# Optimization experiments

Measured on AMD Instinct MI355X. Metric: run time of the kernel, lower is better.

Reference implementation:

```python
import jax, jax.numpy as jnp
import numpy as np

ALPHA = 0.3
B, T, I, H = 256, 1024, 128, 1024


def setup_inputs() -> dict:
    key = jax.random.key(0)
    ks = jax.random.split(key, 7)
    s = 1.0 / np.sqrt(H)
    return {
        "x": jax.random.normal(ks[0], (B, T, I), dtype=jnp.float32),
        "W_ih": jax.random.normal(ks[1], (3 * H, I), dtype=jnp.float32) * s,
        "W_hh": jax.random.normal(ks[2], (3 * H, H), dtype=jnp.float32) * s,
        "b_ih": jax.random.normal(ks[3], (3 * H,), dtype=jnp.float32) * s,
        "b_hh": jax.random.normal(ks[4], (3 * H,), dtype=jnp.float32) * s,
        "W_fc": jax.random.normal(ks[5], (2, H), dtype=jnp.float32) * s,
        "b_fc": jax.random.normal(ks[6], (2,), dtype=jnp.float32) * s,
    }


def _forward(x, W_ih, W_hh, b_ih, b_hh, W_fc, b_fc):
    # --- ES normalize: s_i = (1-a)*x_i + a*s_{i-1}, s_0 = x_0 (in-place EMA) ---
    xs = jnp.swapaxes(x, 0, 1)  # [T, B, I]
    s0 = xs[0]

    def ema_step(s, xi):
        s2 = (1.0 - ALPHA) * xi + ALPHA * s
        return s2, s2

    _, rest = jax.lax.scan(ema_step, s0, xs[1:])
    sm = jnp.concatenate([s0[None], rest], axis=0)  # [T, B, I] smoothed
    st_1 = sm[-1]  # [B, I]

    # --- GRU (single layer, batch_first, h0 = 0); gate order r, z, n ---
    gi = jnp.einsum('tbi,gi->tbg', sm, W_ih) + b_ih  # [T, B, 3H]
    h0 = jnp.zeros((x.shape[0], W_hh.shape[1]), dtype=x.dtype)

    def gru_step(h, gi_t):
        gh = h @ W_hh.T + b_hh  # [B, 3H]
        i_r, i_z, i_n = jnp.split(gi_t, 3, axis=-1)
        h_r, h_z, h_n = jnp.split(gh, 3, axis=-1)
        r = jax.nn.sigmoid(i_r + h_r)
        z = jax.nn.sigmoid(i_z + h_z)
        n = jnp.tanh(i_n + r * h_n)
        h2 = (1.0 - z) * n + z * h
        return h2, None

    h_out, _ = jax.lax.scan(gru_step, h0, gi)  # [B, H]

    out = h_out @ W_fc.T + b_fc  # [B, 2]
    # --- ES denormalize with columns [1, 2] of st_1 ---
    out = (out - ALPHA * st_1[:, 1:3]) / (1.0 - ALPHA)
    return out


def reference(x, W_ih, W_hh, b_ih, b_hh, W_fc, b_fc):
    return _forward(x, W_ih, W_hh, b_ih, b_hh, W_fc, b_fc)
```

## Files before the change

kernel.cpp:

```cpp
#include <hip/hip_runtime.h>

typedef __attribute__((ext_vector_type(4))) float f4;
typedef __attribute__((ext_vector_type(8))) short frag8;
typedef unsigned long long u64;
typedef unsigned int u32;
typedef unsigned short u16;

#define ALPHA 0.3f

#define WHH_OFF   0ull
#define WIH_OFF   6291456ull
#define HBUF_OFF  7077888ull
#define FLG_OFF   8126464ull
#define ST1_OFF   8128512ull
#define ZERO_LEN  1052672ull

__device__ __forceinline__ u16 f2bf(float f) {
  u32 u = __float_as_uint(f);
  u32 r = (u + 0x7FFFu + ((u >> 16) & 1u)) >> 16;
  return (u16)r;
}
__device__ __forceinline__ float bf2f(u16 h) {
  return __uint_as_float(((u32)h) << 16);
}
__device__ __forceinline__ float sigmf(float x) {
  float e = __expf(-fabsf(x));
  float s = 1.0f / (1.0f + e);
  return x >= 0.f ? s : 1.0f - s;
}
__device__ __forceinline__ float tanhf_(float x) {
  float e = __expf(-2.0f * fabsf(x));
  float t = (1.0f - e) / (1.0f + e);
  return x >= 0.f ? t : -t;
}
__device__ __forceinline__ frag8 pack_bf16(f4 a, f4 b) {
  union { u16 h[8]; frag8 f; } u;
  u.h[0] = f2bf(a[0]); u.h[1] = f2bf(a[1]); u.h[2] = f2bf(a[2]); u.h[3] = f2bf(a[3]);
  u.h[4] = f2bf(b[0]); u.h[5] = f2bf(b[1]); u.h[6] = f2bf(b[2]); u.h[7] = f2bf(b[3]);
  return u.f;
}

__global__ void prep_bf16(const float* __restrict__ whh_f32,
                          const float* __restrict__ wih_f32,
                          u16* __restrict__ whh, u16* __restrict__ wih) {
  int i = blockIdx.x * 256 + threadIdx.x;
  const int nhh = 3072 * 1024;
  if (i < nhh) whh[i] = f2bf(whh_f32[i]);
  else         wih[i - nhh] = f2bf(wih_f32[i - nhh]);
}

__global__ __launch_bounds__(256, 1) void gru_kernel(
    const float* __restrict__ x,
    const float* __restrict__ b_ih,
    const float* __restrict__ b_hh,
    const u16* __restrict__ whh,
    const u16* __restrict__ wih,
    u64* __restrict__ hbuf,
    u32* __restrict__ flags,
    float* __restrict__ st1)
{
  __shared__ f4 xbuf[4096];
  __shared__ u16 sbuf[32 * 40];
  const int wg = blockIdx.x;
  const int g = wg >> 5, w = wg & 31;
  const int tid = threadIdx.x;
  const int v = tid >> 6;
  const int l = tid & 63;
  const int lm = l & 15, lq = l >> 4;

  frag8 whhf[8][6];
  frag8 wihf[6];
#pragma unroll
  for (int rt = 0; rt < 6; ++rt) {
    int grow = (rt >> 1) * 1024 + w * 32 + (rt & 1) * 16 + lm;
    wihf[rt] = *(const frag8*)(wih + grow * 128 + v * 32 + lq * 8);
#pragma unroll
    for (int kb = 0; kb < 8; ++kb)
      whhf[kb][rt] = *(const frag8*)(whh + grow * 1024 + v * 256 + kb * 32 + lq * 8);
  }

  const int uc = tid & 31;
  const int ub0 = (tid >> 5) << 2;
  const int colg = w * 32 + uc;
  const float bir = b_ih[colg],         bhr = b_hh[colg];
  const float biz = b_ih[1024 + colg],  bhz = b_hh[1024 + colg];
  const float bin_ = b_ih[2048 + colg], bhn = b_hh[2048 + colg];
  f4 hprev = {0.f, 0.f, 0.f, 0.f};

  f4 e0a, e0b, e1a, e1b;
  const float* xb0 = x + (size_t)(g * 32 + lm) * 131072 + v * 32 + lq * 8;
  const float* xb1 = x + (size_t)(g * 32 + 16 + lm) * 131072 + v * 32 + lq * 8;

  u32* fbase = flags + g * 64;
  const f4 zz = {0.f, 0.f, 0.f, 0.f};
  const float A1 = 1.0f - ALPHA;

  f4 acc[2][6], accn[2][2];

  auto gi_compute = [&](int tt) {
    const float* xp0 = xb0 + (size_t)tt * 128;
    const float* xp1 = xb1 + (size_t)tt * 128;
    f4 xa0 = *(const f4*)xp0, xc0 = *(const f4*)(xp0 + 4);
    f4 xa1 = *(const f4*)xp1, xc1 = *(const f4*)(xp1 + 4);
    if (tt == 0) { e0a = xa0; e0b = xc0; e1a = xa1; e1b = xc1; }
    else {
      e0a = A1 * xa0 + ALPHA * e0a; e0b = A1 * xc0 + ALPHA * e0b;
      e1a = A1 * xa1 + ALPHA * e1a; e1b = A1 * xc1 + ALPHA * e1b;
    }
    frag8 smf0 = pack_bf16(e0a, e0b);
    frag8 smf1 = pack_bf16(e1a, e1b);
#pragma unroll
    for (int bh = 0; bh < 2; ++bh) {
#pragma unroll
      for (int rt = 0; rt < 6; ++rt) acc[bh][rt] = zz;
      accn[bh][0] = zz; accn[bh][1] = zz;
    }
#pragma unroll
    for (int rt = 0; rt < 4; ++rt) {
      acc[0][rt] = __builtin_amdgcn_mfma_f32_16x16x32_bf16(smf0, wihf[rt], acc[0][rt], 0, 0, 0);
      acc[1][rt] = __builtin_amdgcn_mfma_f32_16x16x32_bf16(smf1, wihf[rt], acc[1][rt], 0, 0, 0);
    }
#pragma unroll
    for (int nt = 0; nt < 2; ++nt) {
      accn[0][nt] = __builtin_amdgcn_mfma_f32_16x16x32_bf16(smf0, wihf[4 + nt], accn[0][nt], 0, 0, 0);
      accn[1][nt] = __builtin_amdgcn_mfma_f32_16x16x32_bf16(smf1, wihf[4 + nt], accn[1][nt], 0, 0, 0);
    }
  };

  gi_compute(0);

#pragma unroll 1
  for (int t = 0; t < 1024; ++t) {
    u64* hread  = hbuf + (size_t)((t & 1) * 8 + g) * 8192;
    u64* hwrite = hbuf + (size_t)(((t + 1) & 1) * 8 + g) * 8192;

    frag8 af[8][2];
#pragma unroll
    for (int kb = 0; kb < 8; ++kb) {
#pragma unroll
      for (int bh = 0; bh < 2; ++bh) {
        int base = (((8 * v + kb) * 2 + bh) * 64 + l) * 2;
        union { u64 q[2]; frag8 f; } uu;
        uu.q[0] = __hip_atomic_load(hread + base,     __ATOMIC_RELAXED, __HIP_MEMORY_SCOPE_AGENT);
        uu.q[1] = __hip_atomic_load(hread + base + 1, __ATOMIC_RELAXED, __HIP_MEMORY_SCOPE_AGENT);
        af[kb][bh] = uu.f;
      }
    }
#pragma unroll
    for (int kb = 0; kb < 8; ++kb) {
#pragma unroll
      for (int rt = 0; rt < 6; ++rt) {
        acc[0][rt] = __builtin_amdgcn_mfma_f32_16x16x32_bf16(af[kb][0], whhf[kb][rt], acc[0][rt], 0, 0, 0);
        acc[1][rt] = __builtin_amdgcn_mfma_f32_16x16x32_bf16(af[kb][1], whhf[kb][rt], acc[1][rt], 0, 0, 0);
      }
    }

#pragma unroll
    for (int bh = 0; bh < 2; ++bh) {
      int b8 = bh * 4 + lq;
#pragma unroll
      for (int rt = 0; rt < 6; ++rt) {
        int gr = rt * 16 + lm;
        xbuf[((v * 128 + gr) << 3) | (b8 ^ (gr & 7))] = acc[bh][rt];
      }
#pragma unroll
      for (int nt = 0; nt < 2; ++nt) {
        int gr = 96 + nt * 16 + lm;
        xbuf[((v * 128 + gr) << 3) | (b8 ^ (gr & 7))] = accn[bh][nt];
      }
    }
    __syncthreads();

    int swz = (ub0 >> 2) ^ (uc & 7);
    f4 sr = zz, sz4 = zz, gn4 = zz, gin4 = zz;
#pragma unroll
    for (int vv = 0; vv < 4; ++vv) {
      sr   += xbuf[((vv * 128 + uc) << 3) | swz];
      sz4  += xbuf[((vv * 128 + 32 + uc) << 3) | swz];
      gn4  += xbuf[((vv * 128 + 64 + uc) << 3) | swz];
      gin4 += xbuf[((vv * 128 + 96 + uc) << 3) | swz];
    }
    f4 h4;
#pragma unroll
    for (int i = 0; i < 4; ++i) {
      float rr = sigmf(sr[i] + bir + bhr);
      float zg = sigmf(sz4[i] + biz + bhz);
      float nn = tanhf_(gin4[i] + bin_ + rr * (gn4[i] + bhn));
      h4[i] = (1.0f - zg) * nn + zg * hprev[i];
    }
    hprev = h4;

#pragma unroll
    for (int i = 0; i < 4; ++i) sbuf[(ub0 + i) * 40 + uc] = f2bf(h4[i]);
    __syncthreads();
    {
      int b = tid >> 3, c0 = (tid & 7) << 2;
      u64 pk = *(const u64*)(sbuf + b * 40 + c0);
      int off = ((w * 2 + (b >> 4)) * 64 + (b & 15) + 16 * (c0 >> 3)) * 2 + ((c0 & 7) >> 2);
      __hip_atomic_store(hwrite + off, pk, __ATOMIC_RELAXED, __HIP_MEMORY_SCOPE_AGENT);
    }
    __syncthreads();

    if (tid == 0)
      __hip_atomic_store(fbase + w, (u32)(t + 1), __ATOMIC_RELEASE, __HIP_MEMORY_SCOPE_AGENT);

    if (t < 1023) gi_compute(t + 1);

    if (v == 0) {
      u32 tgt = (u32)(t + 1);
      for (;;) {
        u32 f = __hip_atomic_load(fbase + (l & 31), __ATOMIC_RELAXED, __HIP_MEMORY_SCOPE_AGENT);
        if (__ballot(f < tgt) == 0) break;
        __builtin_amdgcn_s_sleep(1);
      }
      __builtin_amdgcn_fence(__ATOMIC_ACQUIRE, "agent");
    }
    __syncthreads();
  }

  if (w == 0 && v == 0 && lq == 0) {
    st1[(g * 32 + lm) * 2 + 0] = e0a[1];
    st1[(g * 32 + lm) * 2 + 1] = e0a[2];
    st1[(g * 32 + 16 + lm) * 2 + 0] = e1a[1];
    st1[(g * 32 + 16 + lm) * 2 + 1] = e1a[2];
  }
}

__global__ void fc_kernel(const u16* __restrict__ hbuf_bf,
                          const float* __restrict__ wfc,
                          const float* __restrict__ bfc,
                          const float* __restrict__ st1,
                          float* __restrict__ out)
{
  int b = blockIdx.x, t = threadIdx.x;
  int g = b >> 5, bl = b & 31, bh = bl >> 4;
  int k0 = t * 4, kb = k0 >> 5, ko = k0 & 31;
  int lane = (bl & 15) + 16 * (ko >> 3);
  const u16* hp = hbuf_bf + (size_t)g * 32768 + ((kb * 2 + bh) * 64 + lane) * 8 + (ko & 7);
  float h0 = bf2f(hp[0]), h1 = bf2f(hp[1]), h2 = bf2f(hp[2]), h3 = bf2f(hp[3]);
  float s0 = h0 * wfc[k0] + h1 * wfc[k0 + 1] + h2 * wfc[k0 + 2] + h3 * wfc[k0 + 3];
  float s1 = h0 * wfc[1024 + k0] + h1 * wfc[1024 + k0 + 1] +
             h2 * wfc[1024 + k0 + 2] + h3 * wfc[1024 + k0 + 3];
#pragma unroll
  for (int off = 32; off > 0; off >>= 1) {
    s0 += __shfl_down(s0, off);
    s1 += __shfl_down(s1, off);
  }
  __shared__ float red[8];
  if ((t & 63) == 0) { red[(t >> 6) * 2] = s0; red[(t >> 6) * 2 + 1] = s1; }
  __syncthreads();
  if (t == 0) {
    float a0 = red[0] + red[2] + red[4] + red[6] + bfc[0];
    float a1 = red[1] + red[3] + red[5] + red[7] + bfc[1];
    float inv = 1.0f / (1.0f - ALPHA);
    out[b * 2 + 0] = (a0 - ALPHA * st1[b * 2 + 0]) * inv;
    out[b * 2 + 1] = (a1 - ALPHA * st1[b * 2 + 1]) * inv;
  }
}

extern "C" void kernel_launch(void* const* d_in, const int* in_sizes, int n_in,
                              void* d_out, int out_size, void* d_ws, size_t ws_size,
                              hipStream_t stream) {
  const float* x   = (const float*)d_in[0];
  const float* Wih = (const float*)d_in[1];
  const float* Whh = (const float*)d_in[2];
  const float* bih = (const float*)d_in[3];
  const float* bhh = (const float*)d_in[4];
  const float* Wfc = (const float*)d_in[5];
  const float* bfc = (const float*)d_in[6];
  char* ws = (char*)d_ws;
  u16* whh_bf = (u16*)(ws + WHH_OFF);
  u16* wih_bf = (u16*)(ws + WIH_OFF);
  u64* hbuf   = (u64*)(ws + HBUF_OFF);
  u32* flags  = (u32*)(ws + FLG_OFF);
  float* st1  = (float*)(ws + ST1_OFF);

  hipMemsetAsync(ws + HBUF_OFF, 0, ZERO_LEN, stream);
  prep_bf16<<<13824, 256, 0, stream>>>(Whh, Wih, whh_bf, wih_bf);
  gru_kernel<<<256, 256, 0, stream>>>(x, bih, bhh, whh_bf, wih_bf, hbuf, flags, st1);
  fc_kernel<<<256, 256, 0, stream>>>((const u16*)(ws + HBUF_OFF), Wfc, bfc, st1,
                                     (float*)d_out);
}
```

Baseline: 11.53 ms.

## Replace block barrier handoff with per-wave flags and row-major hidden-state layout

The end-of-step barrier handoff is replaced: each wave now publishes its own release flag right after storing its share of the new hidden state, and every wave polls per-wave flags at the start of the next step. The second __syncthreads and the single-thread flag store are gone. The input projection is now computed at the top of each step, before the wait, and the next x row is prefetched. The hidden buffer moves to a plain row-major bf16 layout with 32-bit stores, and fc_kernel reads it accordingly. The aim is to cut barrier latency on the serial recurrence critical path. The risk is 4x more flags to poll, and the acquire fence is replaced by only a compiler barrier, which may weaken memory ordering.

```diff
diff --git a/kernel.cpp b/kernel.cpp
--- a/kernel.cpp
+++ b/kernel.cpp
@@ -12,7 +12,7 @@
 #define WIH_OFF   6291456ull
 #define HBUF_OFF  7077888ull
 #define FLG_OFF   8126464ull
-#define ST1_OFF   8128512ull
+#define ST1_OFF   8130560ull
 #define ZERO_LEN  1052672ull
 
 __device__ __forceinline__ u16 f2bf(float f) {
@@ -55,12 +55,12 @@
     const float* __restrict__ b_hh,
     const u16* __restrict__ whh,
     const u16* __restrict__ wih,
-    u64* __restrict__ hbuf,
+    u16* __restrict__ hbuf,
     u32* __restrict__ flags,
     float* __restrict__ st1)
 {
   __shared__ f4 xbuf[4096];
-  __shared__ u16 sbuf[32 * 40];
+  __shared__ u16 sbuf[1024];
   const int wg = blockIdx.x;
   const int g = wg >> 5, w = wg & 31;
   const int tid = threadIdx.x;
@@ -90,25 +90,32 @@
   f4 e0a, e0b, e1a, e1b;
   const float* xb0 = x + (size_t)(g * 32 + lm) * 131072 + v * 32 + lq * 8;
   const float* xb1 = x + (size_t)(g * 32 + 16 + lm) * 131072 + v * 32 + lq * 8;
-
-  u32* fbase = flags + g * 64;
+  f4 xn0 = *(const f4*)xb0, xn1 = *(const f4*)(xb0 + 4);
+  f4 xn2 = *(const f4*)xb1, xn3 = *(const f4*)(xb1 + 4);
+
+  u32* flg = flags + g * 128;
+  const u32 fidx = v * 32 + (l & 31);
+  const float A1 = 1.0f - ALPHA;
   const f4 zz = {0.f, 0.f, 0.f, 0.f};
-  const float A1 = 1.0f - ALPHA;
-
   f4 acc[2][6], accn[2][2];
 
-  auto gi_compute = [&](int tt) {
-    const float* xp0 = xb0 + (size_t)tt * 128;
-    const float* xp1 = xb1 + (size_t)tt * 128;
-    f4 xa0 = *(const f4*)xp0, xc0 = *(const f4*)(xp0 + 4);
-    f4 xa1 = *(const f4*)xp1, xc1 = *(const f4*)(xp1 + 4);
-    if (tt == 0) { e0a = xa0; e0b = xc0; e1a = xa1; e1b = xc1; }
+#pragma unroll 1
+  for (int t = 0; t < 1024; ++t) {
+    const u64* hr64 = (const u64*)(hbuf + (size_t)((t & 1) * 8 + g) * 32768);
+    u32* hw32 = (u32*)(hbuf + (size_t)(((t + 1) & 1) * 8 + g) * 32768);
+
+    if (t == 0) { e0a = xn0; e0b = xn1; e1a = xn2; e1b = xn3; }
     else {
-      e0a = A1 * xa0 + ALPHA * e0a; e0b = A1 * xc0 + ALPHA * e0b;
-      e1a = A1 * xa1 + ALPHA * e1a; e1b = A1 * xc1 + ALPHA * e1b;
+      e0a = A1 * xn0 + ALPHA * e0a; e0b = A1 * xn1 + ALPHA * e0b;
+      e1a = A1 * xn2 + ALPHA * e1a; e1b = A1 * xn3 + ALPHA * e1b;
     }
     frag8 smf0 = pack_bf16(e0a, e0b);
     frag8 smf1 = pack_bf16(e1a, e1b);
+    {
+      size_t to = (size_t)(t < 1023 ? t + 1 : 1023) * 128;
+      xn0 = *(const f4*)(xb0 + to); xn1 = *(const f4*)(xb0 + to + 4);
+      xn2 = *(const f4*)(xb1 + to); xn3 = *(const f4*)(xb1 + to + 4);
+    }
 #pragma unroll
     for (int bh = 0; bh < 2; ++bh) {
 #pragma unroll
@@ -125,24 +132,26 @@
       accn[0][nt] = __builtin_amdgcn_mfma_f32_16x16x32_bf16(smf0, wihf[4 + nt], accn[0][nt], 0, 0, 0);
       accn[1][nt] = __builtin_amdgcn_mfma_f32_16x16x32_bf16(smf1, wihf[4 + nt], accn[1][nt], 0, 0, 0);
     }
-  };
-
-  gi_compute(0);
-
-#pragma unroll 1
-  for (int t = 0; t < 1024; ++t) {
-    u64* hread  = hbuf + (size_t)((t & 1) * 8 + g) * 8192;
-    u64* hwrite = hbuf + (size_t)(((t + 1) & 1) * 8 + g) * 8192;
+
+    {
+      const u32 tgt = (u32)t;
+      for (;;) {
+        u32 f = __hip_atomic_load(flg + fidx, __ATOMIC_RELAXED, __HIP_MEMORY_SCOPE_AGENT);
+        if (__ballot(f < tgt) == 0ull) break;
+        __builtin_amdgcn_s_sleep(2);
+      }
+      asm volatile("" ::: "memory");
+    }
 
     frag8 af[8][2];
 #pragma unroll
     for (int kb = 0; kb < 8; ++kb) {
 #pragma unroll
       for (int bh = 0; bh < 2; ++bh) {
-        int base = (((8 * v + kb) * 2 + bh) * 64 + l) * 2;
+        const u64* p = hr64 + (bh * 16 + lm) * 256 + (v * 8 + kb) * 8 + lq * 2;
         union { u64 q[2]; frag8 f; } uu;
-        uu.q[0] = __hip_atomic_load(hread + base,     __ATOMIC_RELAXED, __HIP_MEMORY_SCOPE_AGENT);
-        uu.q[1] = __hip_atomic_load(hread + base + 1, __ATOMIC_RELAXED, __HIP_MEMORY_SCOPE_AGENT);
+        uu.q[0] = __hip_atomic_load(p,     __ATOMIC_RELAXED, __HIP_MEMORY_SCOPE_AGENT);
+        uu.q[1] = __hip_atomic_load(p + 1, __ATOMIC_RELAXED, __HIP_MEMORY_SCOPE_AGENT);
         af[kb][bh] = uu.f;
       }
     }
@@ -189,33 +198,20 @@
       h4[i] = (1.0f - zg) * nn + zg * hprev[i];
     }
     hprev = h4;
-
-#pragma unroll
-    for (int i = 0; i < 4; ++i) sbuf[(ub0 + i) * 40 + uc] = f2bf(h4[i]);
+#pragma unroll
+    for (int i = 0; i < 4; ++i) sbuf[(ub0 + i) * 32 + uc] = f2bf(h4[i]);
     __syncthreads();
+
     {
-      int b = tid >> 3, c0 = (tid & 7) << 2;
-      u64 pk = *(const u64*)(sbuf + b * 40 + c0);
-      int off = ((w * 2 + (b >> 4)) * 64 + (b & 15) + 16 * (c0 >> 3)) * 2 + ((c0 & 7) >> 2);
-      __hip_atomic_store(hwrite + off, pk, __ATOMIC_RELAXED, __HIP_MEMORY_SCOPE_AGENT);
-    }
-    __syncthreads();
-
-    if (tid == 0)
-      __hip_atomic_store(fbase + w, (u32)(t + 1), __ATOMIC_RELEASE, __HIP_MEMORY_SCOPE_AGENT);
-
-    if (t < 1023) gi_compute(t + 1);
-
-    if (v == 0) {
-      u32 tgt = (u32)(t + 1);
-      for (;;) {
-        u32 f = __hip_atomic_load(fbase + (l & 31), __ATOMIC_RELAXED, __HIP_MEMORY_SCOPE_AGENT);
-        if (__ballot(f < tgt) == 0) break;
-        __builtin_amdgcn_s_sleep(1);
-      }
-      __builtin_amdgcn_fence(__ATOMIC_ACQUIRE, "agent");
-    }
-    __syncthreads();
+      const u32* s32 = (const u32*)sbuf;
+      u32 a0 = s32[tid], a1 = s32[tid + 256];
+      int b0 = tid >> 4,        c0 = tid & 15;
+      int b1 = (tid + 256) >> 4, c1 = tid & 15;
+      __hip_atomic_store(hw32 + b0 * 512 + w * 16 + c0, a0, __ATOMIC_RELAXED, __HIP_MEMORY_SCOPE_AGENT);
+      __hip_atomic_store(hw32 + b1 * 512 + w * 16 + c1, a1, __ATOMIC_RELAXED, __HIP_MEMORY_SCOPE_AGENT);
+      if (l == 0)
+        __hip_atomic_store(flg + w * 4 + v, (u32)(t + 1), __ATOMIC_RELEASE, __HIP_MEMORY_SCOPE_AGENT);
+    }
   }
 
   if (w == 0 && v == 0 && lq == 0) {
@@ -226,18 +222,18 @@
   }
 }
 
-__global__ void fc_kernel(const u16* __restrict__ hbuf_bf,
+__global__ void fc_kernel(const u16* __restrict__ hbuf,
                           const float* __restrict__ wfc,
                           const float* __restrict__ bfc,
                           const float* __restrict__ st1,
                           float* __restrict__ out)
 {
   int b = blockIdx.x, t = threadIdx.x;
-  int g = b >> 5, bl = b & 31, bh = bl >> 4;
-  int k0 = t * 4, kb = k0 >> 5, ko = k0 & 31;
-  int lane = (bl & 15) + 16 * (ko >> 3);
-  const u16* hp = hbuf_bf + (size_t)g * 32768 + ((kb * 2 + bh) * 64 + lane) * 8 + (ko & 7);
-  float h0 = bf2f(hp[0]), h1 = bf2f(hp[1]), h2 = bf2f(hp[2]), h3 = bf2f(hp[3]);
+  int g = b >> 5, bl = b & 31;
+  int k0 = t * 4;
+  u64 hv = ((const u64*)(hbuf + (size_t)g * 32768))[bl * 256 + t];
+  float h0 = bf2f((u16)(hv & 0xFFFF)),         h1 = bf2f((u16)((hv >> 16) & 0xFFFF));
+  float h2 = bf2f((u16)((hv >> 32) & 0xFFFF)), h3 = bf2f((u16)(hv >> 48));
   float s0 = h0 * wfc[k0] + h1 * wfc[k0 + 1] + h2 * wfc[k0 + 2] + h3 * wfc[k0 + 3];
   float s1 = h0 * wfc[1024 + k0] + h1 * wfc[1024 + k0 + 1] +
              h2 * wfc[1024 + k0 + 2] + h3 * wfc[1024 + k0 + 3];
@@ -271,13 +267,12 @@
   char* ws = (char*)d_ws;
   u16* whh_bf = (u16*)(ws + WHH_OFF);
   u16* wih_bf = (u16*)(ws + WIH_OFF);
-  u64* hbuf   = (u64*)(ws + HBUF_OFF);
+  u16* hbuf   = (u16*)(ws + HBUF_OFF);
   u32* flags  = (u32*)(ws + FLG_OFF);
   float* st1  = (float*)(ws + ST1_OFF);
 
   hipMemsetAsync(ws + HBUF_OFF, 0, ZERO_LEN, stream);
   prep_bf16<<<13824, 256, 0, stream>>>(Whh, Wih, whh_bf, wih_bf);
   gru_kernel<<<256, 256, 0, stream>>>(x, bih, bhh, whh_bf, wih_bf, hbuf, flags, st1);
-  fc_kernel<<<256, 256, 0, stream>>>((const u16*)(ws + HBUF_OFF), Wfc, bfc, st1,
-                                     (float*)d_out);
-}
+  fc_kernel<<<256, 256, 0, stream>>>(hbuf, Wfc, bfc, st1, (float*)d_out);
+}
```

Measured after the change: 21.39 ms. 85.5% more time.
